# Kernel optimization log

Measured on AMD Instinct MI355X. Metric: run time of the kernel, lower is better.

Reference implementation:

```python
import jax, jax.numpy as jnp
import numpy as np

NUM_HEADS = 16
ROT_DIM = 128  # == head_dim here
ROPE_BASE = 10000.0

def _deinterleave(t):
    # non-HF RoPE layout fix: cat(even channels, odd channels) along head_dim
    return jnp.concatenate([t[..., ::2], t[..., 1::2]], axis=-1)

def _rope(t, cos, sin):
    # t: [B,S,H,D]; rotary applied to first ROT_DIM dims with half-split (GPT-NeoX style)
    rot, rest = t[..., :ROT_DIM], t[..., ROT_DIM:]
    x1, x2 = rot[..., : ROT_DIM // 2], rot[..., ROT_DIM // 2 :]
    c = cos[None, :, None, :]
    s = sin[None, :, None, :]
    rot = jnp.concatenate([x1 * c - x2 * s, x1 * s + x2 * c], axis=-1)
    return jnp.concatenate([rot, rest], axis=-1) if rest.shape[-1] else rot

def setup_inputs() -> dict:
    key = jax.random.key(0)
    ks = jax.random.split(key, 5)
    B, S, E = 4, 2048, 2048
    return {
        "x": jax.random.normal(ks[0], (B, S, E), jnp.float32),
        "wqkv_w": jax.random.normal(ks[1], (3 * E, E), jnp.float32) * (E ** -0.5),
        "wqkv_b": jax.random.normal(ks[2], (3 * E,), jnp.float32) * 0.01,
        "wo_w": jax.random.normal(ks[3], (E, E), jnp.float32) * (E ** -0.5),
        "wo_b": jax.random.normal(ks[4], (E,), jnp.float32) * 0.01,
    }

def reference(x, wqkv_w, wqkv_b, wo_w, wo_b):
    B, S, E = x.shape
    H = NUM_HEADS
    D = E // H
    scale = 1.0 / jnp.sqrt(jnp.asarray(D, x.dtype))
    # fused QKV projection; channel layout is (h, three, d)
    qkv = x @ wqkv_w.T + wqkv_b               # [B,S,3E]
    qkv = qkv.reshape(B, S, H, 3, D)
    q, k, v = qkv[..., 0, :], qkv[..., 1, :], qkv[..., 2, :]  # [B,S,H,D]
    # non-HF rotary layout shuffle on q,k only
    q = _deinterleave(q)
    k = _deinterleave(k)
    # rotary embedding
    inv_freq = 1.0 / (ROPE_BASE ** (jnp.arange(0, ROT_DIM, 2, dtype=jnp.float32) / ROT_DIM))
    t = jnp.arange(S, dtype=jnp.float32)
    freqs = jnp.outer(t, inv_freq)            # [S, ROT_DIM/2]
    cos, sin = jnp.cos(freqs).astype(x.dtype), jnp.sin(freqs).astype(x.dtype)
    q = _rope(q, cos, sin)
    k = _rope(k, cos, sin)
    # causal self-attention (vanilla, fp32 softmax)
    scores = jnp.einsum("bshd,bthd->bhst", q, k) * scale   # [B,H,S,S]
    causal = jnp.tril(jnp.ones((S, S), bool))
    scores = jnp.where(causal[None, None], scores, jnp.asarray(-1e4, scores.dtype))
    attn = jax.nn.softmax(scores.astype(jnp.float32), axis=-1).astype(scores.dtype)
    ctx = jnp.einsum("bhst,bthd->bshd", attn, v)           # [B,S,H,D]
    # output projection
    out = ctx.reshape(B, S, E) @ wo_w.T + wo_b
    return out
```

## Files before the change

### kernel.cpp

```cpp
#include <hip/hip_runtime.h>


using frag_ab = __attribute__((ext_vector_type(8))) short;
using frag_cd = __attribute__((ext_vector_type(4))) float;
typedef __attribute__((ext_vector_type(2))) unsigned int uint2v;

__device__ __forceinline__ float b2f(unsigned short u) {
  union { unsigned int i; float f; } v; v.i = ((unsigned int)u) << 16; return v.f;
}
__device__ __forceinline__ unsigned short f2b(float f) {
  union { float f; unsigned int i; } v; v.f = f;
  unsigned int r = v.i + 0x7FFFu + ((v.i >> 16) & 1u);
  return (unsigned short)(r >> 16);
}
__device__ __forceinline__ unsigned int pack2(float a, float b) {
  return (unsigned int)f2b(a) | ((unsigned int)f2b(b) << 16);
}
__device__ __forceinline__ void gload16(const unsigned short* g, unsigned short* l) {
  __builtin_amdgcn_global_load_lds(
      (const __attribute__((address_space(1))) unsigned int*)g,
      (__attribute__((address_space(3))) unsigned int*)l, 16, 0, 0);
}

__global__ __launch_bounds__(256)
void cvt_f32_bf16(const float* __restrict__ in, unsigned short* __restrict__ out) {
  long i = (long)(blockIdx.x * 256 + threadIdx.x) * 8;
  float4 a = *(const float4*)&in[i];
  float4 b = *(const float4*)&in[i + 4];
  uint4 p;
  p.x = pack2(a.x, a.y); p.y = pack2(a.z, a.w);
  p.z = pack2(b.x, b.y); p.w = pack2(b.z, b.w);
  *(uint4*)&out[i] = p;
}

__device__ __forceinline__ void stage_a_async(const unsigned short* A, unsigned short* As,
                                              int row0, int k0, int wave, int lane, int ldk) {
#pragma unroll
  for (int i = 0; i < 4; i++) {
    int rbase = wave * 32 + i * 8;
    int r = rbase + (lane >> 3);
    int srcc = (lane & 7) ^ (r & 7);
    gload16(&A[(long)(row0 + r) * ldk + k0 + srcc * 8], &As[rbase * 64]);
  }
}
__device__ __forceinline__ void stage_b_cvt(const float* Bw, unsigned short* Bs,
                                            int row0, int k0, int tid) {
#pragma unroll
  for (int i = 0; i < 4; i++) {
    int c = tid + i * 256;
    int r = c >> 3, ch = c & 7;
    const float* src = &Bw[(long)(row0 + r) * 2048 + k0 + ch * 8];
    float4 v0 = *(const float4*)src;
    float4 v1 = *(const float4*)(src + 4);
    uint4 p;
    p.x = pack2(v0.x, v0.y); p.y = pack2(v0.z, v0.w);
    p.z = pack2(v1.x, v1.y); p.w = pack2(v1.z, v1.w);
    *(uint4*)&Bs[r * 64 + ((ch ^ (r & 7)) * 8)] = p;
  }
}

__global__ __launch_bounds__(256)
void gemm_qkv(const unsigned short* __restrict__ A,
              const float* __restrict__ Bw,
              const unsigned short* __restrict__ Bbf,
              const float* __restrict__ bias,
              unsigned short* __restrict__ Qb,
              unsigned short* __restrict__ Kb,
              unsigned short* __restrict__ Vt) {
  __shared__ __align__(16) unsigned short As[128 * 64];
  __shared__ __align__(16) unsigned short Bs[128 * 64];
  const int tid  = threadIdx.x;
  const int wave = tid >> 6, lane = tid & 63;
  const int quad = lane >> 4, l16 = lane & 15;
  const int wm = (wave & 1) * 64, wn = (wave >> 1) * 64;
  const int row0A = blockIdx.x * 128;
  const int row0B = blockIdx.y * 128;

  frag_cd acc[4][4];
#pragma unroll
  for (int i = 0; i < 4; i++)
#pragma unroll
    for (int j = 0; j < 4; j++) acc[i][j] = (frag_cd){0.f, 0.f, 0.f, 0.f};

  for (int k0 = 0; k0 < 2048; k0 += 64) {
    stage_a_async(A, As, row0A, k0, wave, lane, 2048);
    if (Bbf) stage_a_async(Bbf, Bs, row0B, k0, wave, lane, 2048);
    else     stage_b_cvt(Bw, Bs, row0B, k0, tid);
    __syncthreads();
#pragma unroll
    for (int kk = 0; kk < 64; kk += 32) {
      frag_ab af[4], bf[4];
#pragma unroll
      for (int mi = 0; mi < 4; mi++) {
        int row = wm + mi * 16 + l16;
        af[mi] = *(const frag_ab*)&As[row * 64 + (((quad + (kk >> 3)) ^ (l16 & 7)) * 8)];
      }
#pragma unroll
      for (int ni = 0; ni < 4; ni++) {
        int row = wn + ni * 16 + l16;
        bf[ni] = *(const frag_ab*)&Bs[row * 64 + (((quad + (kk >> 3)) ^ (l16 & 7)) * 8)];
      }
#pragma unroll
      for (int mi = 0; mi < 4; mi++)
#pragma unroll
        for (int ni = 0; ni < 4; ni++)
          acc[mi][ni] = __builtin_amdgcn_mfma_f32_16x16x32_bf16(af[mi], bf[ni], acc[mi][ni], 0, 0, 0);
    }
    __syncthreads();
  }
#pragma unroll
  for (int ni = 0; ni < 4; ni++) {
    int col  = row0B + wn + ni * 16 + l16;
    int h    = col / 384;
    int rem  = col - h * 384;
    int slot = rem >> 7;
    int d    = rem & 127;
    float bv = bias[col];
#pragma unroll
    for (int mi = 0; mi < 4; mi++) {
#pragma unroll
      for (int r = 0; r < 4; r++) {
        int row = row0A + wm + mi * 16 + quad * 4 + r;
        int b = row >> 11, s = row & 2047;
        unsigned short val = f2b(acc[mi][ni][r] + bv);
        if (slot == 0)      Qb[((long)(b * 16 + h) * 2048 + s) * 128 + d] = val;
        else if (slot == 1) Kb[((long)(b * 16 + h) * 2048 + s) * 128 + d] = val;
        else                Vt[((long)(b * 16 + h) * 128 + d) * 2048 + s] = val;
      }
    }
  }
}

__global__ __launch_bounds__(256)
void rope_inplace(unsigned short* __restrict__ Qb, unsigned short* __restrict__ Kb) {
  int wid  = blockIdx.x * 4 + (threadIdx.x >> 6);
  int j    = threadIdx.x & 63;
  int part = wid & 1;
  int s    = (wid >> 1) & 2047;
  int bh   = wid >> 12;
  unsigned short* buf = part ? Kb : Qb;
  long base = ((long)bh * 2048 + s) * 128;
  unsigned int pr = *(const unsigned int*)&buf[base + 2 * j];
  float x1 = b2f((unsigned short)(pr & 0xFFFFu));
  float x2 = b2f((unsigned short)(pr >> 16));
  float inv = powf(10000.0f, -(float)(2 * j) / 128.0f);
  float ang = (float)s * inv;
  float sn, cs;
  sincosf(ang, &sn, &cs);
  float sc = part ? 1.0f : 0.08838834764831845f;
  cs *= sc; sn *= sc;
  buf[base + j]      = f2b(x1 * cs - x2 * sn);
  buf[base + 64 + j] = f2b(x1 * sn + x2 * cs);
}

__global__ __launch_bounds__(256)
void attn_fwd(const unsigned short* __restrict__ Q,
              const unsigned short* __restrict__ K,
              const unsigned short* __restrict__ Vt,
              unsigned short* __restrict__ ctx) {
  __shared__ __align__(16) unsigned short Ks[64 * 128];
  __shared__ __align__(16) unsigned short Vs[128 * 64];
  __shared__ __align__(16) unsigned short Ps[4][32 * 64];
  const int bh = blockIdx.x;
  const int tid = threadIdx.x;
  const int wave = tid >> 6, lane = tid & 63;
  const int quad = lane >> 4, l16 = lane & 15;
  const long base  = (long)bh * 2048 * 128;
  const long vbase = (long)bh * 262144;
  const int b = bh >> 4, h = bh & 15;
  unsigned short* pw = &Ps[wave][0];

  for (int pass = 0; pass < 2; ++pass) {
    const int qt = pass ? (15 - blockIdx.y) : blockIdx.y;
    const int q0 = qt * 128 + wave * 32;

    frag_ab qf[2][4];
#pragma unroll
    for (int mi = 0; mi < 2; mi++)
#pragma unroll
      for (int ks = 0; ks < 4; ks++)
        qf[mi][ks] = *(const frag_ab*)&Q[base + (long)(q0 + mi * 16 + l16) * 128 + ks * 32 + quad * 8];

    frag_cd o[2][8];
#pragma unroll
    for (int mi = 0; mi < 2; mi++)
#pragma unroll
      for (int ni = 0; ni < 8; ni++) o[mi][ni] = (frag_cd){0.f, 0.f, 0.f, 0.f};
    float m_i[2] = {-1.0e30f, -1.0e30f};
    float l_i[2] = {0.f, 0.f};

    const int kv_end = qt * 128 + 128;
    for (int kv0 = 0; kv0 < kv_end; kv0 += 64) {
      __syncthreads();
#pragma unroll
      for (int i = 0; i < 4; i++) {
        int rbase = (wave * 4 + i) * 4;
        int r = rbase + (lane >> 4);
        int srcc = (lane & 15) ^ (r & 15);
        gload16(&K[base + (long)(kv0 + r) * 128 + srcc * 8], &Ks[rbase * 128]);
      }
#pragma unroll
      for (int i = 0; i < 4; i++) {
        int rbase = wave * 32 + i * 8;
        int r = rbase + (lane >> 3);
        int srcc = (lane & 7) ^ (r & 7);
        gload16(&Vt[vbase + (long)r * 2048 + kv0 + srcc * 8], &Vs[rbase * 64]);
      }
      __syncthreads();

      if (kv0 <= q0 + 31) {
        float p[2][4][4];
        __builtin_amdgcn_s_setprio(1);
#pragma unroll
        for (int kt = 0; kt < 4; kt++) {
          frag_ab kf[4];
          int row = kt * 16 + l16;
#pragma unroll
          for (int ks = 0; ks < 4; ks++)
            kf[ks] = *(const frag_ab*)&Ks[row * 128 + (((ks * 4 + quad) ^ (row & 15)) * 8)];
#pragma unroll
          for (int mi = 0; mi < 2; mi++) {
            frag_cd acc = (frag_cd){0.f, 0.f, 0.f, 0.f};
#pragma unroll
            for (int ks = 0; ks < 4; ks++)
              acc = __builtin_amdgcn_mfma_f32_16x16x32_bf16(kf[ks], qf[mi][ks], acc, 0, 0, 0);
#pragma unroll
            for (int r = 0; r < 4; r++) p[mi][kt][r] = acc[r];
          }
        }
        __builtin_amdgcn_s_setprio(0);

        if (kv0 + 63 > q0) {
#pragma unroll
          for (int mi = 0; mi < 2; mi++) {
            int qg = q0 + mi * 16 + l16;
#pragma unroll
            for (int kt = 0; kt < 4; kt++)
#pragma unroll
              for (int r = 0; r < 4; r++) {
                int kvg = kv0 + kt * 16 + quad * 4 + r;
                if (kvg > qg) p[mi][kt][r] = -10000.0f;
              }
          }
        }

        float alpha[2];
#pragma unroll
        for (int mi = 0; mi < 2; mi++) {
          float mx = -1.0e30f;
#pragma unroll
          for (int kt = 0; kt < 4; kt++)
            mx = fmaxf(mx, fmaxf(fmaxf(p[mi][kt][0], p[mi][kt][1]),
                                 fmaxf(p[mi][kt][2], p[mi][kt][3])));
          mx = fmaxf(mx, __shfl_xor(mx, 16, 64));
          mx = fmaxf(mx, __shfl_xor(mx, 32, 64));
          float mnew = fmaxf(m_i[mi], mx);
          alpha[mi] = __expf(m_i[mi] - mnew);
          m_i[mi] = mnew;
          float rs = 0.f;
#pragma unroll
          for (int kt = 0; kt < 4; kt++)
#pragma unroll
            for (int r = 0; r < 4; r++) {
              float e = __expf(p[mi][kt][r] - mnew);
              p[mi][kt][r] = e;
              rs += e;
            }
          rs += __shfl_xor(rs, 16, 64);
          rs += __shfl_xor(rs, 32, 64);
          l_i[mi] = l_i[mi] * alpha[mi] + rs;
        }

        if (!(__all(alpha[0] == 1.0f) && __all(alpha[1] == 1.0f))) {
#pragma unroll
          for (int mi = 0; mi < 2; mi++) {
            float ar[4];
#pragma unroll
            for (int r = 0; r < 4; r++) ar[r] = __shfl(alpha[mi], quad * 4 + r, 64);
#pragma unroll
            for (int ni = 0; ni < 8; ni++)
#pragma unroll
              for (int r = 0; r < 4; r++) o[mi][ni][r] *= ar[r];
          }
        }

#pragma unroll
        for (int mi = 0; mi < 2; mi++) {
          int row = mi * 16 + l16;
#pragma unroll
          for (int kt = 0; kt < 4; kt++) {
            unsigned int u0 = pack2(p[mi][kt][0], p[mi][kt][1]);
            unsigned int u1 = pack2(p[mi][kt][2], p[mi][kt][3]);
            int ch = kt * 2 + (quad >> 1);
            int addr = row * 64 + ((ch ^ (l16 & 7)) * 8) + (quad & 1) * 4;
            *(uint2v*)&pw[addr] = (uint2v){u0, u1};
          }
        }

        frag_ab pf[2][2];
#pragma unroll
        for (int mi = 0; mi < 2; mi++)
#pragma unroll
          for (int ks = 0; ks < 2; ks++)
            pf[mi][ks] = *(const frag_ab*)&pw[(mi * 16 + l16) * 64 +
                                              (((ks * 4 + quad) ^ (l16 & 7)) * 8)];
        __builtin_amdgcn_s_setprio(1);
#pragma unroll
        for (int ni = 0; ni < 8; ni++) {
          int vrow = ni * 16 + l16;
          frag_ab vf0 = *(const frag_ab*)&Vs[vrow * 64 + ((quad ^ (l16 & 7)) * 8)];
          frag_ab vf1 = *(const frag_ab*)&Vs[vrow * 64 + (((quad + 4) ^ (l16 & 7)) * 8)];
#pragma unroll
          for (int mi = 0; mi < 2; mi++) {
            o[mi][ni] = __builtin_amdgcn_mfma_f32_16x16x32_bf16(pf[mi][0], vf0, o[mi][ni], 0, 0, 0);
            o[mi][ni] = __builtin_amdgcn_mfma_f32_16x16x32_bf16(pf[mi][1], vf1, o[mi][ni], 0, 0, 0);
          }
        }
        __builtin_amdgcn_s_setprio(0);
      }
    }

#pragma unroll
    for (int mi = 0; mi < 2; mi++) {
      float rl = 1.0f / fmaxf(l_i[mi], 1.0e-20f);
#pragma unroll
      for (int r = 0; r < 4; r++) {
        float inv = __shfl(rl, quad * 4 + r, 64);
        int s = q0 + mi * 16 + quad * 4 + r;
        long rowb = ((long)b * 2048 + s) * 2048 + h * 128;
#pragma unroll
        for (int ni = 0; ni < 8; ni++)
          ctx[rowb + ni * 16 + l16] = f2b(o[mi][ni][r] * inv);
      }
    }
  }
}

__global__ __launch_bounds__(256)
void gemm_ctx(const unsigned short* __restrict__ A,
              const float* __restrict__ Bw,
              const unsigned short* __restrict__ Bbf,
              const float* __restrict__ bias,
              float* __restrict__ C) {
  __shared__ __align__(16) unsigned short As[128 * 64];
  __shared__ __align__(16) unsigned short Bs[128 * 64];
  const int tid  = threadIdx.x;
  const int wave = tid >> 6, lane = tid & 63;
  const int quad = lane >> 4, l16 = lane & 15;
  const int wm = (wave & 1) * 64, wn = (wave >> 1) * 64;
  const int row0A = blockIdx.x * 128;
  const int row0B = blockIdx.y * 128;

  frag_cd acc[4][4];
#pragma unroll
  for (int i = 0; i < 4; i++)
#pragma unroll
    for (int j = 0; j < 4; j++) acc[i][j] = (frag_cd){0.f, 0.f, 0.f, 0.f};

  for (int k0 = 0; k0 < 2048; k0 += 64) {
    stage_a_async(A, As, row0A, k0, wave, lane, 2048);
    if (Bbf) stage_a_async(Bbf, Bs, row0B, k0, wave, lane, 2048);
    else     stage_b_cvt(Bw, Bs, row0B, k0, tid);
    __syncthreads();
#pragma unroll
    for (int kk = 0; kk < 64; kk += 32) {
      frag_ab af[4], bf[4];
#pragma unroll
      for (int mi = 0; mi < 4; mi++) {
        int row = wm + mi * 16 + l16;
        af[mi] = *(const frag_ab*)&As[row * 64 + (((quad + (kk >> 3)) ^ (l16 & 7)) * 8)];
      }
#pragma unroll
      for (int ni = 0; ni < 4; ni++) {
        int row = wn + ni * 16 + l16;
        bf[ni] = *(const frag_ab*)&Bs[row * 64 + (((quad + (kk >> 3)) ^ (l16 & 7)) * 8)];
      }
#pragma unroll
      for (int mi = 0; mi < 4; mi++)
#pragma unroll
        for (int ni = 0; ni < 4; ni++)
          acc[mi][ni] = __builtin_amdgcn_mfma_f32_16x16x32_bf16(af[mi], bf[ni], acc[mi][ni], 0, 0, 0);
    }
    __syncthreads();
  }
#pragma unroll
  for (int ni = 0; ni < 4; ni++) {
    int col = row0B + wn + ni * 16 + l16;
    float bv = bias[col];
#pragma unroll
    for (int mi = 0; mi < 4; mi++) {
#pragma unroll
      for (int r = 0; r < 4; r++) {
        int row = row0A + wm + mi * 16 + quad * 4 + r;
        C[(long)row * 2048 + col] = acc[mi][ni][r] + bv;
      }
    }
  }
}

extern "C" void kernel_launch(void* const* d_in, const int* in_sizes, int n_in,
                              void* d_out, int out_size, void* d_ws, size_t ws_size,
                              hipStream_t stream) {
  const float* x      = (const float*)d_in[0];
  const float* wqkv_w = (const float*)d_in[1];
  const float* wqkv_b = (const float*)d_in[2];
  const float* wo_w   = (const float*)d_in[3];
  const float* wo_b   = (const float*)d_in[4];

  unsigned short* xb  = (unsigned short*)d_out;
  unsigned short* Qb  = (unsigned short*)d_out + 16777216;
  unsigned short* Kb  = (unsigned short*)d_ws;
  unsigned short* Vt  = (unsigned short*)d_ws + 16777216;
  unsigned short* ctx = (unsigned short*)d_out;
  float* outf = (float*)d_ws;

  const bool big = ws_size >= 100663296UL;
  unsigned short* Wq = big ? (unsigned short*)d_ws + 33554432 : nullptr;
  unsigned short* Wo = big ? (unsigned short*)d_ws + 46137344 : nullptr;

  cvt_f32_bf16<<<8192, 256, 0, stream>>>(x, xb);
  if (big) {
    cvt_f32_bf16<<<6144, 256, 0, stream>>>(wqkv_w, Wq);
    cvt_f32_bf16<<<2048, 256, 0, stream>>>(wo_w, Wo);
  }
  gemm_qkv<<<dim3(64, 48), 256, 0, stream>>>(xb, wqkv_w, Wq, wqkv_b, Qb, Kb, Vt);
  rope_inplace<<<65536, 256, 0, stream>>>(Qb, Kb);
  attn_fwd<<<dim3(64, 8), 256, 0, stream>>>(Qb, Kb, Vt, ctx);
  gemm_ctx<<<dim3(64, 16), 256, 0, stream>>>(ctx, wo_w, Wo, wo_b, outf);
  hipMemcpyAsync(d_out, outf, 67108864UL, hipMemcpyDeviceToDevice, stream);
}
```

Measured before the change: 735.7 us.

## Add 256x256 double-buffered pipelined GEMM kernels for QKV and output projections

Adds new GEMM kernels with 512 threads, 256x256 tiles, double-buffered LDS and async global-to-LDS loads. Loads for the next K step are interleaved with four MFMA quadrants, using barriers and s_setprio. These kernels replace the old 128x128 single-buffered GEMMs when the bf16 weight copies exist. The aim is to hide load latency and raise data reuse per tile, at the cost of more LDS (128KB per block), more registers and fewer blocks for the output projection (256).

```diff
diff --git a/kernel.cpp b/kernel.cpp
--- a/kernel.cpp
+++ b/kernel.cpp
@@ -31,6 +31,14 @@
   p.x = pack2(a.x, a.y); p.y = pack2(a.z, a.w);
   p.z = pack2(b.x, b.y); p.w = pack2(b.z, b.w);
   *(uint4*)&out[i] = p;
+}
+
+__device__ __forceinline__ void stage_round512(const unsigned short* G, unsigned short* Ls,
+                                               int row0, int k0, int rr0,
+                                               int wave, int lane) {
+  int r = rr0 + wave * 8 + (lane >> 3);
+  int srcc = (lane & 7) ^ (r & 7);
+  gload16(&G[(long)(row0 + r) * 2048 + k0 + srcc * 8], &Ls[(rr0 + wave * 8) * 64]);
 }
 
 __device__ __forceinline__ void stage_a_async(const unsigned short* A, unsigned short* As,
@@ -59,10 +67,185 @@
   }
 }
 
+#define LDA_(mi, ks) (*(const frag_ab*)&as[(wr * 128 + (mi) * 16 + l16) * 64 + ((((ks) * 4 + quad) ^ (l16 & 7)) * 8)])
+#define LDB_(ni, ks) (*(const frag_ab*)&bs[(wc * 64  + (ni) * 16 + l16) * 64 + ((((ks) * 4 + quad) ^ (l16 & 7)) * 8)])
+
+#define GEMM256_BODY(Aptr, Bptr)                                               \
+                                \
+  stage_round512(Aptr, As_[0], row0A, 0, 0,   wave, lane);                     \
+  stage_round512(Aptr, As_[0], row0A, 0, 64,  wave, lane);                     \
+  stage_round512(Aptr, As_[0], row0A, 0, 128, wave, lane);                     \
+  stage_round512(Aptr, As_[0], row0A, 0, 192, wave, lane);                     \
+  stage_round512(Bptr, Bs_[0], row0B, 0, 0,   wave, lane);                     \
+  stage_round512(Bptr, Bs_[0], row0B, 0, 64,  wave, lane);                     \
+  stage_round512(Bptr, Bs_[0], row0B, 0, 128, wave, lane);                     \
+  stage_round512(Bptr, Bs_[0], row0B, 0, 192, wave, lane);                     \
+  stage_round512(Aptr, As_[1], row0A, 64, 0,  wave, lane);                     \
+  stage_round512(Aptr, As_[1], row0A, 64, 64, wave, lane);                     \
+  asm volatile("s_waitcnt vmcnt(2)" ::: "memory");                             \
+  __builtin_amdgcn_s_barrier();                                                \
+  for (int t = 0; t < 32; ++t) {                                               \
+    const int c = t & 1;                                                       \
+    const unsigned short* as = As_[c];                                         \
+    const unsigned short* bs = Bs_[c];                                         \
+    unsigned short* asN = As_[c ^ 1];                                          \
+    unsigned short* bsN = Bs_[c ^ 1];                                          \
+    unsigned short* asC = As_[c];                                              \
+    const int k1 = (t + 1) * 64, k2 = (t + 2) * 64;                            \
+    frag_ab aLo[2][4], aHi[2][4], bLo[2][2], bHi[2][2];                        \
+          \
+    if (t < 31) {                                                              \
+      stage_round512(Aptr, asN, row0A, k1, 128, wave, lane);                   \
+      stage_round512(Aptr, asN, row0A, k1, 192, wave, lane);                   \
+    }                                                                          \
+    _Pragma("unroll") for (int ks = 0; ks < 2; ks++) {                         \
+      _Pragma("unroll") for (int mi = 0; mi < 4; mi++) aLo[ks][mi] = LDA_(mi, ks); \
+      _Pragma("unroll") for (int ni = 0; ni < 2; ni++) bLo[ks][ni] = LDB_(ni, ks); \
+    }                                                                          \
+    __builtin_amdgcn_s_barrier();                                              \
+    __builtin_amdgcn_s_setprio(1);                                             \
+    _Pragma("unroll") for (int ks = 0; ks < 2; ks++)                           \
+      _Pragma("unroll") for (int mi = 0; mi < 4; mi++)                         \
+        _Pragma("unroll") for (int ni = 0; ni < 2; ni++)                       \
+          acc[mi][ni] = __builtin_amdgcn_mfma_f32_16x16x32_bf16(aLo[ks][mi], bLo[ks][ni], acc[mi][ni], 0, 0, 0); \
+    __builtin_amdgcn_s_setprio(0);                                             \
+    __builtin_amdgcn_s_barrier();                                              \
+                \
+    if (t < 31) {                                                              \
+      stage_round512(Bptr, bsN, row0B, k1, 0,  wave, lane);                    \
+      stage_round512(Bptr, bsN, row0B, k1, 64, wave, lane);                    \
+    }                                                                          \
+    _Pragma("unroll") for (int ks = 0; ks < 2; ks++)                           \
+      _Pragma("unroll") for (int ni = 0; ni < 2; ni++) bHi[ks][ni] = LDB_(2 + ni, ks); \
+    __builtin_amdgcn_s_barrier();                                              \
+    __builtin_amdgcn_s_setprio(1);                                             \
+    _Pragma("unroll") for (int ks = 0; ks < 2; ks++)                           \
+      _Pragma("unroll") for (int mi = 0; mi < 4; mi++)                         \
+        _Pragma("unroll") for (int ni = 0; ni < 2; ni++)                       \
+          acc[mi][2 + ni] = __builtin_amdgcn_mfma_f32_16x16x32_bf16(aLo[ks][mi], bHi[ks][ni], acc[mi][2 + ni], 0, 0, 0); \
+    __builtin_amdgcn_s_setprio(0);                                             \
+    __builtin_amdgcn_s_barrier();                                              \
+              \
+    if (t < 31) {                                                              \
+      stage_round512(Bptr, bsN, row0B, k1, 128, wave, lane);                   \
+      stage_round512(Bptr, bsN, row0B, k1, 192, wave, lane);                   \
+    }                                                                          \
+    _Pragma("unroll") for (int ks = 0; ks < 2; ks++)                           \
+      _Pragma("unroll") for (int mi = 0; mi < 4; mi++) aHi[ks][mi] = LDA_(4 + mi, ks); \
+    __builtin_amdgcn_s_barrier();                                              \
+    __builtin_amdgcn_s_setprio(1);                                             \
+    _Pragma("unroll") for (int ks = 0; ks < 2; ks++)                           \
+      _Pragma("unroll") for (int mi = 0; mi < 4; mi++)                         \
+        _Pragma("unroll") for (int ni = 0; ni < 2; ni++)                       \
+          acc[4 + mi][ni] = __builtin_amdgcn_mfma_f32_16x16x32_bf16(aHi[ks][mi], bLo[ks][ni], acc[4 + mi][ni], 0, 0, 0); \
+    __builtin_amdgcn_s_setprio(0);                                             \
+    __builtin_amdgcn_s_barrier();                                              \
+       \
+    if (t < 30) {                                                              \
+      stage_round512(Aptr, asC, row0A, k2, 0,  wave, lane);                    \
+      stage_round512(Aptr, asC, row0A, k2, 64, wave, lane);                    \
+    }                                                                          \
+    __builtin_amdgcn_s_barrier();                                              \
+    __builtin_amdgcn_s_setprio(1);                                             \
+    _Pragma("unroll") for (int ks = 0; ks < 2; ks++)                           \
+      _Pragma("unroll") for (int mi = 0; mi < 4; mi++)                         \
+        _Pragma("unroll") for (int ni = 0; ni < 2; ni++)                       \
+          acc[4 + mi][2 + ni] = __builtin_amdgcn_mfma_f32_16x16x32_bf16(aHi[ks][mi], bHi[ks][ni], acc[4 + mi][2 + ni], 0, 0, 0); \
+    __builtin_amdgcn_s_setprio(0);                                             \
+    if (t < 30)       asm volatile("s_waitcnt vmcnt(2)" ::: "memory");         \
+    else if (t == 30) asm volatile("s_waitcnt vmcnt(0)" ::: "memory");         \
+    __builtin_amdgcn_s_barrier();                                              \
+  }
+
+__global__ __launch_bounds__(512, 2)
+void gemm_qkv2(const unsigned short* __restrict__ A,
+               const unsigned short* __restrict__ Bbf,
+               const float* __restrict__ bias,
+               unsigned short* __restrict__ Qb,
+               unsigned short* __restrict__ Kb,
+               unsigned short* __restrict__ Vt) {
+  __shared__ __align__(16) unsigned short As_[2][256 * 64];
+  __shared__ __align__(16) unsigned short Bs_[2][256 * 64];
+  const int tid  = threadIdx.x;
+  const int wave = tid >> 6, lane = tid & 63;
+  const int quad = lane >> 4, l16 = lane & 15;
+  const int wr = wave >> 2, wc = wave & 3;
+  const int row0A = blockIdx.x * 256;
+  const int row0B = blockIdx.y * 256;
+
+  frag_cd acc[8][4];
+#pragma unroll
+  for (int i = 0; i < 8; i++)
+#pragma unroll
+    for (int j = 0; j < 4; j++) acc[i][j] = (frag_cd){0.f, 0.f, 0.f, 0.f};
+
+  GEMM256_BODY(A, Bbf)
+
+#pragma unroll
+  for (int ni = 0; ni < 4; ni++) {
+    int col  = row0B + wc * 64 + ni * 16 + l16;
+    int h    = col / 384;
+    int rem  = col - h * 384;
+    int slot = rem >> 7;
+    int d    = rem & 127;
+    float bv = bias[col];
+#pragma unroll
+    for (int mi = 0; mi < 8; mi++) {
+#pragma unroll
+      for (int r = 0; r < 4; r++) {
+        int row = row0A + wr * 128 + mi * 16 + quad * 4 + r;
+        int b = row >> 11, s = row & 2047;
+        unsigned short val = f2b(acc[mi][ni][r] + bv);
+        if (slot == 0)      Qb[((long)(b * 16 + h) * 2048 + s) * 128 + d] = val;
+        else if (slot == 1) Kb[((long)(b * 16 + h) * 2048 + s) * 128 + d] = val;
+        else                Vt[((long)(b * 16 + h) * 128 + d) * 2048 + s] = val;
+      }
+    }
+  }
+}
+
+__global__ __launch_bounds__(512, 2)
+void gemm_ctx2(const unsigned short* __restrict__ A,
+               const unsigned short* __restrict__ Bbf,
+               const float* __restrict__ bias,
+               float* __restrict__ C) {
+  __shared__ __align__(16) unsigned short As_[2][256 * 64];
+  __shared__ __align__(16) unsigned short Bs_[2][256 * 64];
+  const int tid  = threadIdx.x;
+  const int wave = tid >> 6, lane = tid & 63;
+  const int quad = lane >> 4, l16 = lane & 15;
+  const int wr = wave >> 2, wc = wave & 3;
+  const int row0A = blockIdx.x * 256;
+  const int row0B = blockIdx.y * 256;
+
+  frag_cd acc[8][4];
+#pragma unroll
+  for (int i = 0; i < 8; i++)
+#pragma unroll
+    for (int j = 0; j < 4; j++) acc[i][j] = (frag_cd){0.f, 0.f, 0.f, 0.f};
+
+  GEMM256_BODY(A, Bbf)
+
+#pragma unroll
+  for (int ni = 0; ni < 4; ni++) {
+    int col = row0B + wc * 64 + ni * 16 + l16;
+    float bv = bias[col];
+#pragma unroll
+    for (int mi = 0; mi < 8; mi++) {
+#pragma unroll
+      for (int r = 0; r < 4; r++) {
+        int row = row0A + wr * 128 + mi * 16 + quad * 4 + r;
+        C[(long)row * 2048 + col] = acc[mi][ni][r] + bv;
+      }
+    }
+  }
+}
+#undef LDA_
+#undef LDB_
+
 __global__ __launch_bounds__(256)
 void gemm_qkv(const unsigned short* __restrict__ A,
               const float* __restrict__ Bw,
-              const unsigned short* __restrict__ Bbf,
               const float* __restrict__ bias,
               unsigned short* __restrict__ Qb,
               unsigned short* __restrict__ Kb,
@@ -84,8 +267,7 @@
 
   for (int k0 = 0; k0 < 2048; k0 += 64) {
     stage_a_async(A, As, row0A, k0, wave, lane, 2048);
-    if (Bbf) stage_a_async(Bbf, Bs, row0B, k0, wave, lane, 2048);
-    else     stage_b_cvt(Bw, Bs, row0B, k0, tid);
+    stage_b_cvt(Bw, Bs, row0B, k0, tid);
     __syncthreads();
 #pragma unroll
     for (int kk = 0; kk < 64; kk += 32) {
@@ -339,7 +521,6 @@
 __global__ __launch_bounds__(256)
 void gemm_ctx(const unsigned short* __restrict__ A,
               const float* __restrict__ Bw,
-              const unsigned short* __restrict__ Bbf,
               const float* __restrict__ bias,
               float* __restrict__ C) {
   __shared__ __align__(16) unsigned short As[128 * 64];
@@ -359,8 +540,7 @@
 
   for (int k0 = 0; k0 < 2048; k0 += 64) {
     stage_a_async(A, As, row0A, k0, wave, lane, 2048);
-    if (Bbf) stage_a_async(Bbf, Bs, row0B, k0, wave, lane, 2048);
-    else     stage_b_cvt(Bw, Bs, row0B, k0, tid);
+    stage_b_cvt(Bw, Bs, row0B, k0, tid);
     __syncthreads();
 #pragma unroll
     for (int kk = 0; kk < 64; kk += 32) {
@@ -423,9 +603,11 @@
     cvt_f32_bf16<<<6144, 256, 0, stream>>>(wqkv_w, Wq);
     cvt_f32_bf16<<<2048, 256, 0, stream>>>(wo_w, Wo);
   }
-  gemm_qkv<<<dim3(64, 48), 256, 0, stream>>>(xb, wqkv_w, Wq, wqkv_b, Qb, Kb, Vt);
+  if (big) gemm_qkv2<<<dim3(32, 24), 512, 0, stream>>>(xb, Wq, wqkv_b, Qb, Kb, Vt);
+  else     gemm_qkv<<<dim3(64, 48), 256, 0, stream>>>(xb, wqkv_w, wqkv_b, Qb, Kb, Vt);
   rope_inplace<<<65536, 256, 0, stream>>>(Qb, Kb);
   attn_fwd<<<dim3(64, 8), 256, 0, stream>>>(Qb, Kb, Vt, ctx);
-  gemm_ctx<<<dim3(64, 16), 256, 0, stream>>>(ctx, wo_w, Wo, wo_b, outf);
+  if (big) gemm_ctx2<<<dim3(32, 8), 512, 0, stream>>>(ctx, Wo, wo_b, outf);
+  else     gemm_ctx<<<dim3(64, 16), 256, 0, stream>>>(ctx, wo_w, wo_b, outf);
   hipMemcpyAsync(d_out, outf, 67108864UL, hipMemcpyDeviceToDevice, stream);
 }
```

Measured after the change: 779.8 us. +6.0%, slower.

## Double-buffer K/V tiles in attention and precompute RoPE cos/sin table

Applied to the files above, without the earlier changes.

The attention kernel now keeps two LDS buffers for the K and V tiles and issues the async global-to-LDS load of the next tile before computing on the current one, with a single barrier per iteration. This is meant to hide global memory latency behind the MFMA work. Separately, RoPE cos/sin values are computed once into a small table (placed in d_out, which xb no longer needs after the QKV GEMM), so the per-element powf/sincosf calls go away. The double buffering doubles K/V LDS usage, which may lower occupancy.

```diff
diff --git a/kernel.cpp b/kernel.cpp
--- a/kernel.cpp
+++ b/kernel.cpp
@@ -132,7 +132,19 @@
 }
 
 __global__ __launch_bounds__(256)
-void rope_inplace(unsigned short* __restrict__ Qb, unsigned short* __restrict__ Kb) {
+void rope_tab(float2* __restrict__ tab) {
+  int i = blockIdx.x * 256 + threadIdx.x;
+  int s = i >> 6, j = i & 63;
+  float inv = powf(10000.0f, -(float)(2 * j) / 128.0f);
+  float ang = (float)s * inv;
+  float sn, cs;
+  sincosf(ang, &sn, &cs);
+  tab[i] = make_float2(cs, sn);
+}
+
+__global__ __launch_bounds__(256)
+void rope_inplace(unsigned short* __restrict__ Qb, unsigned short* __restrict__ Kb,
+                  const float2* __restrict__ tab) {
   int wid  = blockIdx.x * 4 + (threadIdx.x >> 6);
   int j    = threadIdx.x & 63;
   int part = wid & 1;
@@ -143,14 +155,32 @@
   unsigned int pr = *(const unsigned int*)&buf[base + 2 * j];
   float x1 = b2f((unsigned short)(pr & 0xFFFFu));
   float x2 = b2f((unsigned short)(pr >> 16));
-  float inv = powf(10000.0f, -(float)(2 * j) / 128.0f);
-  float ang = (float)s * inv;
-  float sn, cs;
-  sincosf(ang, &sn, &cs);
+  float2 t = tab[s * 64 + j];
   float sc = part ? 1.0f : 0.08838834764831845f;
-  cs *= sc; sn *= sc;
+  float cs = t.x * sc, sn = t.y * sc;
   buf[base + j]      = f2b(x1 * cs - x2 * sn);
   buf[base + 64 + j] = f2b(x1 * sn + x2 * cs);
+}
+
+__device__ __forceinline__ void attn_stage(const unsigned short* __restrict__ K,
+                                           const unsigned short* __restrict__ Vt,
+                                           long base, long vbase, int kv0,
+                                           unsigned short* Kbuf, unsigned short* Vbuf,
+                                           int wave, int lane) {
+#pragma unroll
+  for (int i = 0; i < 4; i++) {
+    int rbase = (wave * 4 + i) * 4;
+    int r = rbase + (lane >> 4);
+    int srcc = (lane & 15) ^ (r & 15);
+    gload16(&K[base + (long)(kv0 + r) * 128 + srcc * 8], &Kbuf[rbase * 128]);
+  }
+#pragma unroll
+  for (int i = 0; i < 4; i++) {
+    int rbase = wave * 32 + i * 8;
+    int r = rbase + (lane >> 3);
+    int srcc = (lane & 7) ^ (r & 7);
+    gload16(&Vt[vbase + (long)r * 2048 + kv0 + srcc * 8], &Vbuf[rbase * 64]);
+  }
 }
 
 __global__ __launch_bounds__(256)
@@ -158,8 +188,8 @@
               const unsigned short* __restrict__ K,
               const unsigned short* __restrict__ Vt,
               unsigned short* __restrict__ ctx) {
-  __shared__ __align__(16) unsigned short Ks[64 * 128];
-  __shared__ __align__(16) unsigned short Vs[128 * 64];
+  __shared__ __align__(16) unsigned short Ks[2][64 * 128];
+  __shared__ __align__(16) unsigned short Vs[2][128 * 64];
   __shared__ __align__(16) unsigned short Ps[4][32 * 64];
   const int bh = blockIdx.x;
   const int tid = threadIdx.x;
@@ -189,26 +219,19 @@
     float m_i[2] = {-1.0e30f, -1.0e30f};
     float l_i[2] = {0.f, 0.f};
 
-    const int kv_end = qt * 128 + 128;
-    for (int kv0 = 0; kv0 < kv_end; kv0 += 64) {
-      __syncthreads();
-#pragma unroll
-      for (int i = 0; i < 4; i++) {
-        int rbase = (wave * 4 + i) * 4;
-        int r = rbase + (lane >> 4);
-        int srcc = (lane & 15) ^ (r & 15);
-        gload16(&K[base + (long)(kv0 + r) * 128 + srcc * 8], &Ks[rbase * 128]);
-      }
-#pragma unroll
-      for (int i = 0; i < 4; i++) {
-        int rbase = wave * 32 + i * 8;
-        int r = rbase + (lane >> 3);
-        int srcc = (lane & 7) ^ (r & 7);
-        gload16(&Vt[vbase + (long)r * 2048 + kv0 + srcc * 8], &Vs[rbase * 64]);
-      }
-      __syncthreads();
+    const int nt = qt * 2 + 2;
+    attn_stage(K, Vt, base, vbase, 0, Ks[0], Vs[0], wave, lane);
+    __syncthreads();
+
+    for (int t = 0; t < nt; ++t) {
+      const int kv0 = t * 64;
+      const int c = t & 1;
+      if (t + 1 < nt)
+        attn_stage(K, Vt, base, vbase, kv0 + 64, Ks[c ^ 1], Vs[c ^ 1], wave, lane);
 
       if (kv0 <= q0 + 31) {
+        const unsigned short* ks_ = Ks[c];
+        const unsigned short* vs_ = Vs[c];
         float p[2][4][4];
         __builtin_amdgcn_s_setprio(1);
 #pragma unroll
@@ -217,7 +240,7 @@
           int row = kt * 16 + l16;
 #pragma unroll
           for (int ks = 0; ks < 4; ks++)
-            kf[ks] = *(const frag_ab*)&Ks[row * 128 + (((ks * 4 + quad) ^ (row & 15)) * 8)];
+            kf[ks] = *(const frag_ab*)&ks_[row * 128 + (((ks * 4 + quad) ^ (row & 15)) * 8)];
 #pragma unroll
           for (int mi = 0; mi < 2; mi++) {
             frag_cd acc = (frag_cd){0.f, 0.f, 0.f, 0.f};
@@ -308,8 +331,8 @@
 #pragma unroll
         for (int ni = 0; ni < 8; ni++) {
           int vrow = ni * 16 + l16;
-          frag_ab vf0 = *(const frag_ab*)&Vs[vrow * 64 + ((quad ^ (l16 & 7)) * 8)];
-          frag_ab vf1 = *(const frag_ab*)&Vs[vrow * 64 + (((quad + 4) ^ (l16 & 7)) * 8)];
+          frag_ab vf0 = *(const frag_ab*)&vs_[vrow * 64 + ((quad ^ (l16 & 7)) * 8)];
+          frag_ab vf1 = *(const frag_ab*)&vs_[vrow * 64 + (((quad + 4) ^ (l16 & 7)) * 8)];
 #pragma unroll
           for (int mi = 0; mi < 2; mi++) {
             o[mi][ni] = __builtin_amdgcn_mfma_f32_16x16x32_bf16(pf[mi][0], vf0, o[mi][ni], 0, 0, 0);
@@ -318,6 +341,7 @@
         }
         __builtin_amdgcn_s_setprio(0);
       }
+      __syncthreads();
     }
 
 #pragma unroll
@@ -412,6 +436,7 @@
   unsigned short* Kb  = (unsigned short*)d_ws;
   unsigned short* Vt  = (unsigned short*)d_ws + 16777216;
   unsigned short* ctx = (unsigned short*)d_out;
+  float2* tab = (float2*)d_out;
   float* outf = (float*)d_ws;
 
   const bool big = ws_size >= 100663296UL;
@@ -424,7 +449,8 @@
     cvt_f32_bf16<<<2048, 256, 0, stream>>>(wo_w, Wo);
   }
   gemm_qkv<<<dim3(64, 48), 256, 0, stream>>>(xb, wqkv_w, Wq, wqkv_b, Qb, Kb, Vt);
-  rope_inplace<<<65536, 256, 0, stream>>>(Qb, Kb);
+  rope_tab<<<512, 256, 0, stream>>>(tab);
+  rope_inplace<<<65536, 256, 0, stream>>>(Qb, Kb, tab);
   attn_fwd<<<dim3(64, 8), 256, 0, stream>>>(Qb, Kb, Vt, ctx);
   gemm_ctx<<<dim3(64, 16), 256, 0, stream>>>(ctx, wo_w, Wo, wo_b, outf);
   hipMemcpyAsync(d_out, outf, 67108864UL, hipMemcpyDeviceToDevice, stream);
```

Measured after the change: 712.3 us. 1.03x faster.
